# Optimization experiments

Measured on AMD Instinct MI355X. Metric: run time of the kernel, lower is better.

The kernel has to match this reference:

```python
import jax, jax.numpy as jnp
import numpy as np

D_MODEL = 2048
N_HEADS = 32
N_KV_HEADS = 8
HEAD_DIM = D_MODEL // N_HEADS          # 64
GROUP = N_HEADS // N_KV_HEADS          # 4
B, T = 1, 2048
SWA_WINDOW = 512


def _rope_tables(T, half_dim):
    # standard RoPE frequencies, theta=10000
    inv_freq = 1.0 / (10000.0 ** (np.arange(half_dim, dtype=np.float32) / half_dim))
    pos = np.arange(T, dtype=np.float32)
    ang = pos[:, None] * inv_freq[None, :]          # [T, D/2]
    return jnp.asarray(np.sin(ang)), jnp.asarray(np.cos(ang))


def setup_inputs() -> dict:
    key = jax.random.key(0)
    ks = jax.random.split(key, 5)
    scale = 1.0 / np.sqrt(D_MODEL)
    x = jax.random.normal(ks[0], (B, T, D_MODEL), dtype=jnp.float32)
    Wq = jax.random.normal(ks[1], (D_MODEL, N_HEADS * HEAD_DIM), dtype=jnp.float32) * scale
    Wk = jax.random.normal(ks[2], (D_MODEL, N_KV_HEADS * HEAD_DIM), dtype=jnp.float32) * scale
    Wv = jax.random.normal(ks[3], (D_MODEL, N_KV_HEADS * HEAD_DIM), dtype=jnp.float32) * scale
    Wo = jax.random.normal(ks[4], (N_HEADS * HEAD_DIM, D_MODEL), dtype=jnp.float32) * scale
    rope_sin, rope_cos = _rope_tables(T, HEAD_DIM // 2)
    return {"x": x, "Wq": Wq, "Wk": Wk, "Wv": Wv, "Wo": Wo,
            "rope_sin": rope_sin, "rope_cos": rope_cos, "swa_window": SWA_WINDOW}


def apply_rope(x, sin, cos):
    # x: [B, T, H, D]; sin/cos: [T, D/2], interleaved-pair rotation in fp32
    orig_dtype = x.dtype
    Bx, Tx, Hx, Dx = x.shape
    xf = x.astype(jnp.float32).reshape(Bx, Tx, Hx, Dx // 2, 2)
    x1, x2 = xf[..., 0], xf[..., 1]
    s = sin.astype(jnp.float32)[None, :, None, :]
    c = cos.astype(jnp.float32)[None, :, None, :]
    out = jnp.stack((x1 * c - x2 * s, x1 * s + x2 * c), axis=-1)
    return out.reshape(Bx, Tx, Hx, Dx).astype(orig_dtype)


def reference(x, Wq, Wk, Wv, Wo, rope_sin, rope_cos, swa_window):
    Bx, Tx, C = x.shape
    q = (x @ Wq).reshape(Bx, Tx, N_HEADS, HEAD_DIM)
    k = (x @ Wk).reshape(Bx, Tx, N_KV_HEADS, HEAD_DIM)
    v = (x @ Wv).reshape(Bx, Tx, N_KV_HEADS, HEAD_DIM)

    q = apply_rope(q, rope_sin, rope_cos)
    k = apply_rope(k, rope_sin, rope_cos)

    # repeat_interleave KV heads to match query heads (GQA)
    k = jnp.repeat(k, GROUP, axis=2)   # [B, T, H, D]
    v = jnp.repeat(v, GROUP, axis=2)

    q = q.transpose(0, 2, 1, 3)        # [B, H, T, D]
    k = k.transpose(0, 2, 1, 3)
    v = v.transpose(0, 2, 1, 3)

    # causal + sliding-window mask: disallow j > i or i - j > swa_window
    idx = jnp.arange(Tx)
    delta = idx[:, None] - idx[None, :]          # [T, T], i - j
    disallowed = delta < 0
    if swa_window > 0:
        disallowed = disallowed | (delta > swa_window)

    scale = 1.0 / np.sqrt(HEAD_DIM)
    scores = jnp.einsum('bhqd,bhkd->bhqk', q, k) * scale
    scores = jnp.where(disallowed[None, None], -jnp.inf, scores)
    weights = jax.nn.softmax(scores, axis=-1)
    attn = jnp.einsum('bhqk,bhkd->bhqd', weights, v)   # [B, H, T, D]

    attn = attn.transpose(0, 2, 1, 3).reshape(Bx, Tx, C)
    return attn @ Wo
```

## Files before the change

kernel.cpp:

```cpp
#include <hip/hip_runtime.h>
#include <math.h>

#define DMODEL 2048
#define NH     32
#define NKV    8
#define HDIM   64
#define GROUP  4
#define KVW    (NKV * HDIM)

typedef short bf16x8 __attribute__((ext_vector_type(8)));
typedef float f32x4  __attribute__((ext_vector_type(4)));

__device__ __forceinline__ short f2bf(float f) {
    union { float f; unsigned u; } x; x.f = f;
    unsigned r = x.u + 0x7fffu + ((x.u >> 16) & 1u);
    return (short)(r >> 16);
}
__device__ __forceinline__ float bf2f(short h) {
    union { unsigned u; float f; } x; x.u = ((unsigned)(unsigned short)h) << 16;
    return x.f;
}

typedef __attribute__((address_space(3))) void lds_void;
typedef const __attribute__((address_space(1))) void gbl_void;
__device__ __forceinline__ void gll16(const void* g, void* l) {
    __builtin_amdgcn_global_load_lds((gbl_void*)g, (lds_void*)l, 16, 0, 0);
}

__global__ __launch_bounds__(256)
void split_f32(const float* __restrict__ in, short* __restrict__ oh,
               short* __restrict__ ol, int n4)
{
    int i = blockIdx.x * 256 + threadIdx.x;
    if (i >= n4) return;
    float4 v = ((const float4*)in)[i];
    short h0 = f2bf(v.x), h1 = f2bf(v.y), h2 = f2bf(v.z), h3 = f2bf(v.w);
    short l0 = f2bf(v.x - bf2f(h0)), l1 = f2bf(v.y - bf2f(h1));
    short l2 = f2bf(v.z - bf2f(h2)), l3 = f2bf(v.w - bf2f(h3));
    ((short4*)oh)[i] = make_short4(h0, h1, h2, h3);
    ((short4*)ol)[i] = make_short4(l0, l1, l2, l3);
}

__global__ __launch_bounds__(256)
void transpose_split_f32(const float* __restrict__ W, int K, int N,
                         short* __restrict__ oth, short* __restrict__ otl, int ldo)
{
    __shared__ float tile[32][33];
    const int bx = blockIdx.x, by = blockIdx.y;
    const int c = threadIdx.x & 31, r = threadIdx.x >> 5;
    #pragma unroll
    for (int it = 0; it < 4; ++it)
        tile[r + it * 8][c] = W[(size_t)(by * 32 + r + it * 8) * N + bx * 32 + c];
    __syncthreads();
    #pragma unroll
    for (int it = 0; it < 4; ++it) {
        int n = bx * 32 + r + it * 8;
        int k = by * 32 + c;
        float v = tile[c][r + it * 8];
        short h = f2bf(v), l = f2bf(v - bf2f(h));
        oth[(size_t)n * ldo + k] = h;
        otl[(size_t)n * ldo + k] = l;
    }
}

__global__ __launch_bounds__(256)
void transpose_bf16(const short* __restrict__ in, int R, int C,
                    short* __restrict__ out)
{
    __shared__ short tile[32][33];
    const int bx = blockIdx.x, by = blockIdx.y;
    const int c = threadIdx.x & 31, r = threadIdx.x >> 5;
    #pragma unroll
    for (int it = 0; it < 4; ++it)
        tile[r + it * 8][c] = in[(size_t)(by * 32 + r + it * 8) * C + bx * 32 + c];
    __syncthreads();
    #pragma unroll
    for (int it = 0; it < 4; ++it)
        out[(size_t)(bx * 32 + r + it * 8) * R + by * 32 + c] = tile[c][r + it * 8];
}

template <int MODE>
__global__ __launch_bounds__(256)
void gemm3(const short* __restrict__ Ah, const short* __restrict__ Al,
           const short* __restrict__ Bh, const short* __restrict__ Bl,
           int K,
           float* __restrict__ C, int ldc,
           short* __restrict__ Qo, short* __restrict__ Ko, short* __restrict__ Vo,
           const float* __restrict__ rs, const float* __restrict__ rc)
{
    __shared__ __align__(16) short AhS[128 * 32];
    __shared__ __align__(16) short AlS[128 * 32];
    __shared__ __align__(16) short BhS[128 * 32];
    __shared__ __align__(16) short BlS[128 * 32];

    const int t = threadIdx.x, lane = t & 63, w = t >> 6;
    const int wr = (w >> 1) * 64, wc = (w & 1) * 64;
    const int m0 = blockIdx.y * 128, n0 = blockIdx.x * 128;

    f32x4 zero = {0.f, 0.f, 0.f, 0.f};
    f32x4 acc[4][4];
    #pragma unroll
    for (int i = 0; i < 4; ++i)
        #pragma unroll
        for (int j = 0; j < 4; ++j) acc[i][j] = zero;

    const int sr0 = (w * 2 + 0) * 16 + (lane >> 2);
    const int sr1 = (w * 2 + 1) * 16 + (lane >> 2);
    const int sc0 = (((lane & 3) ^ (sr0 & 3)) * 8);
    const int sc1 = (((lane & 3) ^ (sr1 & 3)) * 8);
    const size_t ga0 = (size_t)(m0 + sr0) * K + sc0;
    const size_t ga1 = (size_t)(m0 + sr1) * K + sc1;
    const size_t gb0 = (size_t)(n0 + sr0) * K + sc0;
    const size_t gb1 = (size_t)(n0 + sr1) * K + sc1;
    char* lA0 = (char*)AhS + (w * 2 + 0) * 1024;
    char* lA1 = (char*)AhS + (w * 2 + 1) * 1024;
    char* lAl0 = (char*)AlS + (w * 2 + 0) * 1024;
    char* lAl1 = (char*)AlS + (w * 2 + 1) * 1024;
    char* lB0 = (char*)BhS + (w * 2 + 0) * 1024;
    char* lB1 = (char*)BhS + (w * 2 + 1) * 1024;
    char* lBl0 = (char*)BlS + (w * 2 + 0) * 1024;
    char* lBl1 = (char*)BlS + (w * 2 + 1) * 1024;

    const int fr = lane & 15, fs = lane >> 4;

    for (int k0 = 0; k0 < K; k0 += 32) {
        __syncthreads();
        gll16(Ah + ga0 + k0, lA0);
        gll16(Ah + ga1 + k0, lA1);
        gll16(Al + ga0 + k0, lAl0);
        gll16(Al + ga1 + k0, lAl1);
        gll16(Bh + gb0 + k0, lB0);
        gll16(Bh + gb1 + k0, lB1);
        gll16(Bl + gb0 + k0, lBl0);
        gll16(Bl + gb1 + k0, lBl1);
        __syncthreads();

        bf16x8 fah[4], fal[4], fbh[4], fbl[4];
        #pragma unroll
        for (int i = 0; i < 4; ++i) {
            int ar = wr + i * 16 + fr;
            int aoff = ar * 64 + ((fs ^ (ar & 3)) << 4);
            fah[i] = *(const bf16x8*)((const char*)AhS + aoff);
            fal[i] = *(const bf16x8*)((const char*)AlS + aoff);
            int br = wc + i * 16 + fr;
            int boff = br * 64 + ((fs ^ (br & 3)) << 4);
            fbh[i] = *(const bf16x8*)((const char*)BhS + boff);
            fbl[i] = *(const bf16x8*)((const char*)BlS + boff);
        }
        #pragma unroll
        for (int i = 0; i < 4; ++i)
            #pragma unroll
            for (int j = 0; j < 4; ++j) {
                acc[i][j] = __builtin_amdgcn_mfma_f32_16x16x32_bf16(fah[i], fbh[j], acc[i][j], 0, 0, 0);
                acc[i][j] = __builtin_amdgcn_mfma_f32_16x16x32_bf16(fah[i], fbl[j], acc[i][j], 0, 0, 0);
                acc[i][j] = __builtin_amdgcn_mfma_f32_16x16x32_bf16(fal[i], fbh[j], acc[i][j], 0, 0, 0);
            }
    }

    const int g = lane >> 4;
    #pragma unroll
    for (int i = 0; i < 4; ++i)
        #pragma unroll
        for (int j = 0; j < 4; ++j)
            #pragma unroll
            for (int r = 0; r < 4; ++r) {
                int m = m0 + wr + i * 16 + g * 4 + r;
                int n = n0 + wc + j * 16 + fr;
                float v = acc[i][j][r];
                if (MODE == 0) {
                    C[(size_t)m * ldc + n] = v;
                } else {
                    if (n < 2048 + 512) {
                        float p = __shfl_xor(v, 1);
                        int pi = (n & (HDIM - 1)) >> 1;
                        float sn = rs[m * (HDIM / 2) + pi];
                        float cs = rc[m * (HDIM / 2) + pi];
                        v = ((lane & 1) == 0) ? (v * cs - p * sn) : (p * sn + v * cs);
                    }
                    short b = f2bf(v);
                    if (n < 2048)            Qo[(size_t)m * DMODEL + n] = b;
                    else if (n < 2048 + 512) Ko[(size_t)m * KVW + (n - 2048)] = b;
                    else                     Vo[(size_t)m * KVW + (n - 2560)] = b;
                }
            }
}

__global__ __launch_bounds__(256)
void attn_mfma(const short* __restrict__ Qb, const short* __restrict__ Kb,
               const short* __restrict__ Vt, short* __restrict__ AoH,
               short* __restrict__ AoL, const int* __restrict__ swa_ptr, int T)
{
    __shared__ __align__(16) short Ks[32 * 64];
    __shared__ __align__(16) short Vs[64 * 32];
    __shared__ __align__(16) short Ps[4][16 * 32];

    const int h = blockIdx.y, qt = blockIdx.x;
    const int q0 = qt * 64, hk = h >> 2;
    const int t = threadIdx.x, lane = t & 63, w = t >> 6;
    const int swa = *swa_ptr;
    const int fr = lane & 15, g = lane >> 4;
    const int qrow = q0 + w * 16;

    bf16x8 qf0, qf1;
    {
        const short* qp = Qb + (size_t)(qrow + fr) * DMODEL + h * HDIM + g * 8;
        qf0 = *(const bf16x8*)qp;
        qf1 = *(const bf16x8*)(qp + 32);
    }

    f32x4 zero = {0.f, 0.f, 0.f, 0.f};
    f32x4 oacc[4];
    #pragma unroll
    for (int dt = 0; dt < 4; ++dt) oacc[dt] = zero;
    float mreg[4] = {-INFINITY, -INFINITY, -INFINITY, -INFINITY};
    float lreg[4] = {0.f, 0.f, 0.f, 0.f};

    int kt_lo = 0;
    if (swa > 0) { int lo = q0 - swa; if (lo > 0) kt_lo = lo >> 5; }
    const int kt_hi = (q0 + 63) >> 5;

    const int krow = w * 8 + (lane >> 3);
    const int kcol = (((lane & 7) ^ (krow & 7)) * 8);
    const size_t kgbase = (size_t)krow * KVW + hk * HDIM + kcol;
    const int vrow = w * 16 + (lane >> 2);
    const int vcol = (((lane & 3) ^ (vrow & 3)) * 8);
    const size_t vgbase = (size_t)(hk * HDIM + vrow) * T + vcol;

    for (int kt = kt_lo; kt <= kt_hi; ++kt) {
        const int k0 = kt * 32;
        __syncthreads();
        gll16(Kb + (size_t)k0 * KVW + kgbase, (char*)Ks + w * 1024);
        gll16(Vt + vgbase + k0, (char*)Vs + w * 1024);
        __syncthreads();

        f32x4 s0a = zero, s1a = zero;
        #pragma unroll
        for (int ks = 0; ks < 2; ++ks) {
            int slot = g + ks * 4;
            int key0 = fr, key1 = 16 + fr;
            bf16x8 kf0 = *(const bf16x8*)((const char*)Ks + key0 * 128 + ((slot ^ (key0 & 7)) << 4));
            bf16x8 kf1 = *(const bf16x8*)((const char*)Ks + key1 * 128 + ((slot ^ (key1 & 7)) << 4));
            bf16x8 qf = ks ? qf1 : qf0;
            s0a = __builtin_amdgcn_mfma_f32_16x16x32_bf16(qf, kf0, s0a, 0, 0, 0);
            s1a = __builtin_amdgcn_mfma_f32_16x16x32_bf16(qf, kf1, s1a, 0, 0, 0);
        }

        float alpha[4], p0v[4], p1v[4];
        #pragma unroll
        for (int r = 0; r < 4; ++r) {
            int i = qrow + g * 4 + r;
            int j0 = k0 + fr, j1 = k0 + 16 + fr;
            int d0 = i - j0, d1 = i - j1;
            float s0 = (d0 >= 0 && (swa <= 0 || d0 <= swa)) ? s0a[r] * 0.125f : -INFINITY;
            float s1 = (d1 >= 0 && (swa <= 0 || d1 <= swa)) ? s1a[r] * 0.125f : -INFINITY;
            float rm = fmaxf(s0, s1);
            rm = fmaxf(rm, __shfl_xor(rm, 1));
            rm = fmaxf(rm, __shfl_xor(rm, 2));
            rm = fmaxf(rm, __shfl_xor(rm, 4));
            rm = fmaxf(rm, __shfl_xor(rm, 8));
            float mo = mreg[r];
            float mn = fmaxf(mo, rm);
            float a, p0, p1;
            if (mn == -INFINITY) { a = 1.f; p0 = 0.f; p1 = 0.f; }
            else {
                a  = __expf(mo - mn);
                p0 = __expf(s0 - mn);
                p1 = __expf(s1 - mn);
            }
            float rsum = p0 + p1;
            rsum += __shfl_xor(rsum, 1);
            rsum += __shfl_xor(rsum, 2);
            rsum += __shfl_xor(rsum, 4);
            rsum += __shfl_xor(rsum, 8);
            mreg[r] = mn;
            lreg[r] = lreg[r] * a + rsum;
            alpha[r] = a;
            p0v[r] = p0;
            p1v[r] = p1;
        }

        #pragma unroll
        for (int r = 0; r < 4; ++r) {
            int row = g * 4 + r;
            int c0 = fr, c1 = 16 + fr;
            *(short*)((char*)Ps[w] + row * 64 + (((c0 >> 3) ^ (row & 3)) << 4) + ((c0 & 7) << 1)) = f2bf(p0v[r]);
            *(short*)((char*)Ps[w] + row * 64 + (((c1 >> 3) ^ (row & 3)) << 4) + ((c1 & 7) << 1)) = f2bf(p1v[r]);
        }
        __syncthreads();

        #pragma unroll
        for (int dt = 0; dt < 4; ++dt)
            #pragma unroll
            for (int r = 0; r < 4; ++r) oacc[dt][r] = oacc[dt][r] * alpha[r];

        {
            int prow = fr;
            bf16x8 pf = *(const bf16x8*)((const char*)Ps[w] + prow * 64 + ((g ^ (prow & 3)) << 4));
            #pragma unroll
            for (int dt = 0; dt < 4; ++dt) {
                int d = dt * 16 + fr;
                bf16x8 vf = *(const bf16x8*)((const char*)Vs + d * 64 + ((g ^ (d & 3)) << 4));
                oacc[dt] = __builtin_amdgcn_mfma_f32_16x16x32_bf16(pf, vf, oacc[dt], 0, 0, 0);
            }
        }
    }

    float invl[4];
    #pragma unroll
    for (int r = 0; r < 4; ++r) invl[r] = 1.0f / lreg[r];
    #pragma unroll
    for (int dt = 0; dt < 4; ++dt)
        #pragma unroll
        for (int r = 0; r < 4; ++r) {
            int i = qrow + g * 4 + r;
            float v = oacc[dt][r] * invl[r];
            int col = h * HDIM + dt * 16 + fr;
            short hb = f2bf(v);
            short lb = f2bf(v - bf2f(hb));
            AoH[(size_t)i * DMODEL + col] = hb;
            AoL[(size_t)i * DMODEL + col] = lb;
        }
}

extern "C" void kernel_launch(void* const* d_in, const int* in_sizes, int n_in,
                              void* d_out, int out_size, void* d_ws, size_t ws_size,
                              hipStream_t stream)
{
    const float* x    = (const float*)d_in[0];
    const float* Wq   = (const float*)d_in[1];
    const float* Wk   = (const float*)d_in[2];
    const float* Wv   = (const float*)d_in[3];
    const float* Wo   = (const float*)d_in[4];
    const float* rsin = (const float*)d_in[5];
    const float* rcos = (const float*)d_in[6];
    const int*   swa  = (const int*)d_in[7];

    const int T = in_sizes[0] / DMODEL;

    char* p = (char*)d_ws;
    short* WTh  = (short*)p; p += (size_t)3072 * 2048 * 2;
    short* WTl  = (short*)p; p += (size_t)3072 * 2048 * 2;
    short* WoTh = (short*)p; p += (size_t)2048 * 2048 * 2;
    short* WoTl = (short*)p; p += (size_t)2048 * 2048 * 2;
    short* Xh   = (short*)p; p += (size_t)T * DMODEL * 2;
    short* Xl   = (short*)p; p += (size_t)T * DMODEL * 2;
    short* Qbf  = (short*)p; p += (size_t)T * DMODEL * 2;
    short* Kbf  = (short*)p; p += (size_t)T * KVW * 2;
    short* Vbf  = (short*)p; p += (size_t)T * KVW * 2;
    short* Vt   = (short*)p; p += (size_t)T * KVW * 2;
    short* AoH  = Xh;
    short* AoL  = Xl;

    int n4 = T * DMODEL / 4;
    split_f32<<<(n4 + 255) / 256, 256, 0, stream>>>(x, Xh, Xl, n4);

    transpose_split_f32<<<dim3(2048 / 32, 2048 / 32), 256, 0, stream>>>(Wq, 2048, 2048, WTh, WTl, 2048);
    transpose_split_f32<<<dim3(512 / 32, 2048 / 32), 256, 0, stream>>>(Wk, 2048, 512, WTh + (size_t)2048 * 2048, WTl + (size_t)2048 * 2048, 2048);
    transpose_split_f32<<<dim3(512 / 32, 2048 / 32), 256, 0, stream>>>(Wv, 2048, 512, WTh + (size_t)2560 * 2048, WTl + (size_t)2560 * 2048, 2048);
    transpose_split_f32<<<dim3(2048 / 32, 2048 / 32), 256, 0, stream>>>(Wo, 2048, 2048, WoTh, WoTl, 2048);

    gemm3<1><<<dim3(3072 / 128, T / 128), 256, 0, stream>>>(
        Xh, Xl, WTh, WTl, 2048, nullptr, 0, Qbf, Kbf, Vbf, rsin, rcos);

    transpose_bf16<<<dim3(KVW / 32, T / 32), 256, 0, stream>>>(Vbf, T, KVW, Vt);

    attn_mfma<<<dim3(T / 64, NH), 256, 0, stream>>>(Qbf, Kbf, Vt, AoH, AoL, swa, T);

    gemm3<0><<<dim3(2048 / 128, T / 128), 256, 0, stream>>>(
        AoH, AoL, WoTh, WoTl, 2048, (float*)d_out, 2048, nullptr, nullptr, nullptr, nullptr, nullptr);
}
```

Measured before the change: 371.6 us.

## Double-buffer LDS tiles in GEMM and attention, skip masking on full tiles

Both the split-bf16 GEMM and the attention kernel now keep two LDS buffers. The next K-step or KV tile is issued with global-to-LDS loads before the current one is computed, so each iteration needs one barrier instead of two and global latency can overlap the MFMA work. The attention kernel also skips the per-element causal/window mask for tiles that are wholly inside the allowed region. It drops the block-wide barrier after the per-warp P writes, since only the same wave reads that buffer. LDS use doubles, which may lower occupancy.

```diff
diff --git a/kernel.cpp b/kernel.cpp
--- a/kernel.cpp
+++ b/kernel.cpp
@@ -88,10 +88,10 @@
            short* __restrict__ Qo, short* __restrict__ Ko, short* __restrict__ Vo,
            const float* __restrict__ rs, const float* __restrict__ rc)
 {
-    __shared__ __align__(16) short AhS[128 * 32];
-    __shared__ __align__(16) short AlS[128 * 32];
-    __shared__ __align__(16) short BhS[128 * 32];
-    __shared__ __align__(16) short BlS[128 * 32];
+    __shared__ __align__(16) short AhS[2][128 * 32];
+    __shared__ __align__(16) short AlS[2][128 * 32];
+    __shared__ __align__(16) short BhS[2][128 * 32];
+    __shared__ __align__(16) short BlS[2][128 * 32];
 
     const int t = threadIdx.x, lane = t & 63, w = t >> 6;
     const int wr = (w >> 1) * 64, wc = (w & 1) * 64;
@@ -112,40 +112,41 @@
     const size_t ga1 = (size_t)(m0 + sr1) * K + sc1;
     const size_t gb0 = (size_t)(n0 + sr0) * K + sc0;
     const size_t gb1 = (size_t)(n0 + sr1) * K + sc1;
-    char* lA0 = (char*)AhS + (w * 2 + 0) * 1024;
-    char* lA1 = (char*)AhS + (w * 2 + 1) * 1024;
-    char* lAl0 = (char*)AlS + (w * 2 + 0) * 1024;
-    char* lAl1 = (char*)AlS + (w * 2 + 1) * 1024;
-    char* lB0 = (char*)BhS + (w * 2 + 0) * 1024;
-    char* lB1 = (char*)BhS + (w * 2 + 1) * 1024;
-    char* lBl0 = (char*)BlS + (w * 2 + 0) * 1024;
-    char* lBl1 = (char*)BlS + (w * 2 + 1) * 1024;
+    const int co0 = (w * 2 + 0) * 1024;
+    const int co1 = (w * 2 + 1) * 1024;
 
     const int fr = lane & 15, fs = lane >> 4;
 
-    for (int k0 = 0; k0 < K; k0 += 32) {
+    auto stage = [&](int k0, int p) {
+        gll16(Ah + ga0 + k0, (char*)AhS[p] + co0);
+        gll16(Ah + ga1 + k0, (char*)AhS[p] + co1);
+        gll16(Al + ga0 + k0, (char*)AlS[p] + co0);
+        gll16(Al + ga1 + k0, (char*)AlS[p] + co1);
+        gll16(Bh + gb0 + k0, (char*)BhS[p] + co0);
+        gll16(Bh + gb1 + k0, (char*)BhS[p] + co1);
+        gll16(Bl + gb0 + k0, (char*)BlS[p] + co0);
+        gll16(Bl + gb1 + k0, (char*)BlS[p] + co1);
+    };
+
+    const int nsteps = K >> 5;
+    stage(0, 0);
+
+    for (int s = 0; s < nsteps; ++s) {
+        const int p = s & 1;
         __syncthreads();
-        gll16(Ah + ga0 + k0, lA0);
-        gll16(Ah + ga1 + k0, lA1);
-        gll16(Al + ga0 + k0, lAl0);
-        gll16(Al + ga1 + k0, lAl1);
-        gll16(Bh + gb0 + k0, lB0);
-        gll16(Bh + gb1 + k0, lB1);
-        gll16(Bl + gb0 + k0, lBl0);
-        gll16(Bl + gb1 + k0, lBl1);
-        __syncthreads();
+        if (s + 1 < nsteps) stage((s + 1) << 5, p ^ 1);
 
         bf16x8 fah[4], fal[4], fbh[4], fbl[4];
         #pragma unroll
         for (int i = 0; i < 4; ++i) {
             int ar = wr + i * 16 + fr;
             int aoff = ar * 64 + ((fs ^ (ar & 3)) << 4);
-            fah[i] = *(const bf16x8*)((const char*)AhS + aoff);
-            fal[i] = *(const bf16x8*)((const char*)AlS + aoff);
+            fah[i] = *(const bf16x8*)((const char*)AhS[p] + aoff);
+            fal[i] = *(const bf16x8*)((const char*)AlS[p] + aoff);
             int br = wc + i * 16 + fr;
             int boff = br * 64 + ((fs ^ (br & 3)) << 4);
-            fbh[i] = *(const bf16x8*)((const char*)BhS + boff);
-            fbl[i] = *(const bf16x8*)((const char*)BlS + boff);
+            fbh[i] = *(const bf16x8*)((const char*)BhS[p] + boff);
+            fbl[i] = *(const bf16x8*)((const char*)BlS[p] + boff);
         }
         #pragma unroll
         for (int i = 0; i < 4; ++i)
@@ -171,11 +172,11 @@
                     C[(size_t)m * ldc + n] = v;
                 } else {
                     if (n < 2048 + 512) {
-                        float p = __shfl_xor(v, 1);
+                        float pp = __shfl_xor(v, 1);
                         int pi = (n & (HDIM - 1)) >> 1;
                         float sn = rs[m * (HDIM / 2) + pi];
                         float cs = rc[m * (HDIM / 2) + pi];
-                        v = ((lane & 1) == 0) ? (v * cs - p * sn) : (p * sn + v * cs);
+                        v = ((lane & 1) == 0) ? (v * cs - pp * sn) : (pp * sn + v * cs);
                     }
                     short b = f2bf(v);
                     if (n < 2048)            Qo[(size_t)m * DMODEL + n] = b;
@@ -190,8 +191,8 @@
                const short* __restrict__ Vt, short* __restrict__ AoH,
                short* __restrict__ AoL, const int* __restrict__ swa_ptr, int T)
 {
-    __shared__ __align__(16) short Ks[32 * 64];
-    __shared__ __align__(16) short Vs[64 * 32];
+    __shared__ __align__(16) short Ks[2][32 * 64];
+    __shared__ __align__(16) short Vs[2][64 * 32];
     __shared__ __align__(16) short Ps[4][16 * 32];
 
     const int h = blockIdx.y, qt = blockIdx.x;
@@ -226,33 +227,47 @@
     const int vcol = (((lane & 3) ^ (vrow & 3)) * 8);
     const size_t vgbase = (size_t)(hk * HDIM + vrow) * T + vcol;
 
+    auto stage = [&](int kt, int p) {
+        gll16(Kb + (size_t)(kt * 32) * KVW + kgbase, (char*)Ks[p] + w * 1024);
+        gll16(Vt + vgbase + kt * 32, (char*)Vs[p] + w * 1024);
+    };
+
+    stage(kt_lo, 0);
+
     for (int kt = kt_lo; kt <= kt_hi; ++kt) {
         const int k0 = kt * 32;
+        const int p = (kt - kt_lo) & 1;
         __syncthreads();
-        gll16(Kb + (size_t)k0 * KVW + kgbase, (char*)Ks + w * 1024);
-        gll16(Vt + vgbase + k0, (char*)Vs + w * 1024);
-        __syncthreads();
+        if (kt + 1 <= kt_hi) stage(kt + 1, p ^ 1);
 
         f32x4 s0a = zero, s1a = zero;
         #pragma unroll
         for (int ks = 0; ks < 2; ++ks) {
             int slot = g + ks * 4;
             int key0 = fr, key1 = 16 + fr;
-            bf16x8 kf0 = *(const bf16x8*)((const char*)Ks + key0 * 128 + ((slot ^ (key0 & 7)) << 4));
-            bf16x8 kf1 = *(const bf16x8*)((const char*)Ks + key1 * 128 + ((slot ^ (key1 & 7)) << 4));
+            bf16x8 kf0 = *(const bf16x8*)((const char*)Ks[p] + key0 * 128 + ((slot ^ (key0 & 7)) << 4));
+            bf16x8 kf1 = *(const bf16x8*)((const char*)Ks[p] + key1 * 128 + ((slot ^ (key1 & 7)) << 4));
             bf16x8 qf = ks ? qf1 : qf0;
             s0a = __builtin_amdgcn_mfma_f32_16x16x32_bf16(qf, kf0, s0a, 0, 0, 0);
             s1a = __builtin_amdgcn_mfma_f32_16x16x32_bf16(qf, kf1, s1a, 0, 0, 0);
         }
 
+        const bool full = (k0 + 31 <= qrow) && (swa <= 0 || (qrow + 15 - k0) <= swa);
+
         float alpha[4], p0v[4], p1v[4];
         #pragma unroll
         for (int r = 0; r < 4; ++r) {
-            int i = qrow + g * 4 + r;
-            int j0 = k0 + fr, j1 = k0 + 16 + fr;
-            int d0 = i - j0, d1 = i - j1;
-            float s0 = (d0 >= 0 && (swa <= 0 || d0 <= swa)) ? s0a[r] * 0.125f : -INFINITY;
-            float s1 = (d1 >= 0 && (swa <= 0 || d1 <= swa)) ? s1a[r] * 0.125f : -INFINITY;
+            float s0, s1;
+            if (full) {
+                s0 = s0a[r] * 0.125f;
+                s1 = s1a[r] * 0.125f;
+            } else {
+                int i = qrow + g * 4 + r;
+                int j0 = k0 + fr, j1 = k0 + 16 + fr;
+                int d0 = i - j0, d1 = i - j1;
+                s0 = (d0 >= 0 && (swa <= 0 || d0 <= swa)) ? s0a[r] * 0.125f : -INFINITY;
+                s1 = (d1 >= 0 && (swa <= 0 || d1 <= swa)) ? s1a[r] * 0.125f : -INFINITY;
+            }
             float rm = fmaxf(s0, s1);
             rm = fmaxf(rm, __shfl_xor(rm, 1));
             rm = fmaxf(rm, __shfl_xor(rm, 2));
@@ -286,7 +301,6 @@
             *(short*)((char*)Ps[w] + row * 64 + (((c0 >> 3) ^ (row & 3)) << 4) + ((c0 & 7) << 1)) = f2bf(p0v[r]);
             *(short*)((char*)Ps[w] + row * 64 + (((c1 >> 3) ^ (row & 3)) << 4) + ((c1 & 7) << 1)) = f2bf(p1v[r]);
         }
-        __syncthreads();
 
         #pragma unroll
         for (int dt = 0; dt < 4; ++dt)
@@ -299,7 +313,7 @@
             #pragma unroll
             for (int dt = 0; dt < 4; ++dt) {
                 int d = dt * 16 + fr;
-                bf16x8 vf = *(const bf16x8*)((const char*)Vs + d * 64 + ((g ^ (d & 3)) << 4));
+                bf16x8 vf = *(const bf16x8*)((const char*)Vs[p] + d * 64 + ((g ^ (d & 3)) << 4));
                 oacc[dt] = __builtin_amdgcn_mfma_f32_16x16x32_bf16(pf, vf, oacc[dt], 0, 0, 0);
             }
         }
```

Result: faster. 354.3 us (-4.7%).
